# Performance work log

Measured on AMD Instinct MI355X. Metric: run time of the kernel, lower is better.

The kernel has to match this reference:

```python
import jax, jax.numpy as jnp
import numpy as np
from jax import lax

B, L, M, K, H, C = 16, 512, 2, 48, 128, 128
DIN = H * 2 + H + H + C  # 2 hidden layers + seq embed + mutant embed + edge feats = 640
H1, H2 = 512, 256
EPS = 1e-6


def _dist(Ca, mask, top_k=K, eps=EPS):
    # Ca: [B,L,3], mask: [B,L]
    m2 = mask[:, None, :] * mask[:, :, None]                                  # [B,L,L]
    D = m2 * jnp.sqrt(jnp.sum((Ca[:, :, None] - Ca[:, None, :]) ** 2, -1) + eps)
    D_adj = D + (1.0 - m2) * jnp.max(D, -1, keepdims=True)
    negD, E_idx = lax.top_k(-D_adj, top_k)                                    # smallest distances
    return -negD, E_idx


def reference(X, S, mask, chain_M, residue_idx, chain_encoding_all,
              mut_positions, mut_wildtype_AAs, mut_mutant_AAs, mut_ddGs, atom_mask,
              hid1, hid2, mpnn_embed, mpnn_edges, Ws, ln_g, ln_b,
              W1, b1, W2, b2, W3, b3):
    bidx = jnp.arange(B)[:, None]
    # _check_sequence_match: force S to wildtype at mutated positions
    S = S.at[bidx, mut_positions].set(mut_wildtype_AAs)
    X = jnp.nan_to_num(X, nan=0.0)

    # top-k neighbor graph from Ca coords
    _, E_idx = _dist(X[:, :, 1, :], mask)                                     # [B,L,K]

    # gather neighbor lists / edge features at mutation positions
    E_sel = jnp.take_along_axis(E_idx, mut_positions[:, :, None], axis=1)     # [B,M,K]
    Ed_sel = jnp.take_along_axis(mpnn_edges, mut_positions[:, :, None, None], axis=1)  # [B,M,K,C]

    # for each mutation, find edge to each other mutation (first match in neighbor list),
    # nanmean over others (missing -> excluded; all missing -> 0)
    edge_aggs = []
    for m in range(M):
        acc = jnp.zeros((B, C), mpnn_edges.dtype)
        cnt = jnp.zeros((B, 1), mpnn_edges.dtype)
        for o in range(M):
            if o == m:
                continue
            match = E_sel[:, m, :] == mut_positions[:, o, None]               # [B,K]
            has = jnp.any(match, -1)
            idx = jnp.argmax(match, -1)                                       # first occurrence
            edge = jnp.take_along_axis(Ed_sel[:, m], idx[:, None, None], axis=1)[:, 0]  # [B,C]
            acc = acc + edge * has[:, None].astype(edge.dtype)
            cnt = cnt + has[:, None].astype(edge.dtype)
        edge_aggs.append(acc / jnp.maximum(cnt, 1.0))
    edge_agg = jnp.stack(edge_aggs, axis=1)                                   # [B,M,C]

    # per-residue mpnn features and gathers at mutation positions
    h = jnp.concatenate([hid1, hid2, mpnn_embed], -1)                         # [B,L,384]
    g = jnp.take_along_axis(h, mut_positions[:, :, None], axis=1)             # [B,M,384]
    mut_e = Ws[mut_mutant_AAs]                                                # [B,M,H]
    emb = jnp.concatenate([g, mut_e, edge_agg], -1)                           # [B,M,DIN]

    # aggregate over valid mutations (padding has pos+wt+mut == 0)
    valid = ((mut_mutant_AAs + mut_wildtype_AAs + mut_positions) != 0).astype(emb.dtype)[:, :, None]
    agg = jnp.sum(emb * valid, axis=1) / jnp.maximum(jnp.sum(valid, axis=1), 1.0)  # [B,DIN]

    # ddg_out: LayerNorm -> (ReLU, Linear) x3
    mu = jnp.mean(agg, -1, keepdims=True)
    var = jnp.mean((agg - mu) ** 2, -1, keepdims=True)
    y = (agg - mu) / jnp.sqrt(var + 1e-5) * ln_g + ln_b
    y = jax.nn.relu(y) @ W1 + b1
    y = jax.nn.relu(y) @ W2 + b2
    y = jax.nn.relu(y) @ W3 + b3                                              # [B,1]
    return y


def setup_inputs() -> dict:
    key = jax.random.key(0)
    ks = jax.random.split(key, 16)
    f = lambda i, shp, s=1.0: jax.random.normal(ks[i], shp, dtype=jnp.float32) * s
    return {
        "X": f(0, (B, L, 4, 3), 5.0),
        "S": jax.random.randint(ks[1], (B, L), 0, 21),
        "mask": jnp.ones((B, L), jnp.float32),
        "chain_M": jnp.ones((B, L), jnp.float32),
        "residue_idx": jnp.tile(jnp.arange(L)[None, :], (B, 1)),
        "chain_encoding_all": jnp.zeros((B, L), jnp.int32),
        "mut_positions": jax.random.randint(ks[2], (B, M), 0, L),
        "mut_wildtype_AAs": jax.random.randint(ks[3], (B, M), 0, 21),
        "mut_mutant_AAs": jax.random.randint(ks[4], (B, M), 0, 21),
        "mut_ddGs": f(5, (B, M)),
        "atom_mask": jnp.ones((B, L, 4), jnp.float32),
        "hid1": f(6, (B, L, H)),
        "hid2": f(7, (B, L, H)),
        "mpnn_embed": f(8, (B, L, H)),
        "mpnn_edges": f(9, (B, L, K, C), 0.1),
        "Ws": f(10, (21, H), 0.02),
        "ln_g": jnp.ones((DIN,), jnp.float32),
        "ln_b": jnp.zeros((DIN,), jnp.float32),
        "W1": f(11, (DIN, H1), 0.02), "b1": jnp.zeros((H1,), jnp.float32),
        "W2": f(12, (H1, H2), 0.02), "b2": jnp.zeros((H2,), jnp.float32),
        "W3": f(13, (H2, 1), 0.02), "b3": jnp.zeros((1,), jnp.float32),
    }
```

## Files before the change

kernel.cpp:

```cpp
#include <hip/hip_runtime.h>
#include <hip/hip_bf16.h>

#define BB   16
#define LL   512
#define KNB  48
#define DIN_ 640
#define H1_  512
#define H2_  256
#define NT   512

__device__ __forceinline__ float nz(float x) { return x == x ? x : 0.0f; }

__device__ __forceinline__ float wave_sum(float v) {
  #pragma unroll
  for (int m = 32; m >= 1; m >>= 1) v += __shfl_xor(v, m);
  return v;
}

__global__ __launch_bounds__(NT) void k_fused(
    const float* __restrict__ X,
    const int*   __restrict__ mpos,
    const int*   __restrict__ mwt,
    const int*   __restrict__ mmut,
    const float* __restrict__ hid1,
    const float* __restrict__ hid2,
    const float* __restrict__ memb,
    const float* __restrict__ edges,
    const float* __restrict__ Wse,
    const float* __restrict__ ln_g,
    const float* __restrict__ ln_b,
    const float* __restrict__ W1,
    const float* __restrict__ b1,
    const float* __restrict__ W2,
    const float* __restrict__ b2,
    const float* __restrict__ W3,
    const float* __restrict__ b3,
    float* __restrict__ out)
{
  const int b   = blockIdx.x;
  const int t   = threadIdx.x;
  const int wid = t >> 6;

  __shared__ float s_x0[DIN_];
  __shared__ float s_x1[H1_];
  __shared__ float s_p2[NT];
  __shared__ float s_w[24];
  __shared__ int   s_cnt[16];

  const int p[2]  = { mpos[b * 2 + 0], mpos[b * 2 + 1] };
  const int mu[2] = { mmut[b * 2 + 0], mmut[b * 2 + 1] };
  const int wt[2] = { mwt[b * 2 + 0],  mwt[b * 2 + 1]  };

  float3 ca[2];
  #pragma unroll
  for (int m = 0; m < 2; ++m) {
    const float* a = X + (((size_t)(b * LL + p[m])) * 4 + 1) * 3;
    ca[m] = make_float3(nz(a[0]), nz(a[1]), nz(a[2]));
  }

  {
    const float* a = X + (((size_t)(b * LL + t)) * 4 + 1) * 3;
    const float jx = nz(a[0]), jy = nz(a[1]), jz = nz(a[2]);
    const float dx = ca[0].x - ca[1].x, dy = ca[0].y - ca[1].y, dz = ca[0].z - ca[1].z;
    const float dq = sqrtf(dx * dx + dy * dy + dz * dz + 1e-6f);

    const float e0x = jx - ca[0].x, e0y = jy - ca[0].y, e0z = jz - ca[0].z;
    const float d0  = sqrtf(e0x * e0x + e0y * e0y + e0z * e0z + 1e-6f);
    const float e1x = jx - ca[1].x, e1y = jy - ca[1].y, e1z = jz - ca[1].z;
    const float d1  = sqrtf(e1x * e1x + e1y * e1y + e1z * e1z + 1e-6f);

    const bool pr0 = (d0 < dq) || (d0 == dq && t < p[1]);
    const bool pr1 = (d1 < dq) || (d1 == dq && t < p[0]);
    const unsigned long long m0 = __ballot(pr0);
    const unsigned long long m1 = __ballot(pr1);
    if ((t & 63) == 0) {
      s_cnt[wid]     = __popcll(m0);
      s_cnt[8 + wid] = __popcll(m1);
    }
  }
  __syncthreads();

  int rk[2] = { 0, 0 };
  #pragma unroll
  for (int w = 0; w < 8; ++w) { rk[0] += s_cnt[w]; rk[1] += s_cnt[8 + w]; }

  const int v0 = ((p[0] + wt[0] + mu[0]) != 0) ? 1 : 0;
  const int v1 = ((p[1] + wt[1] + mu[1]) != 0) ? 1 : 0;
  const float denom = fmaxf((float)(v0 + v1), 1.0f);
  const int vv[2] = { v0, v1 };

  {
    const int d = t;
    if (true) {
      float v = 0.0f;
      #pragma unroll
      for (int m = 0; m < 2; ++m) {
        if (!vv[m]) continue;
        const int base = p[m];
        float e;
        if (d < 128)      e = hid1[(size_t)(b * LL + base) * 128 + d];
        else if (d < 256) e = hid2[(size_t)(b * LL + base) * 128 + (d - 128)];
        else if (d < 384) e = memb[(size_t)(b * LL + base) * 128 + (d - 256)];
        else              e = Wse[mu[m] * 128 + (d - 384)];
        v += e;
      }
      s_x0[d] = v / denom;
    }
    if (t < DIN_ - NT) {
      const int d = NT + t;
      float v = 0.0f;
      #pragma unroll
      for (int m = 0; m < 2; ++m) {
        if (!vv[m]) continue;
        if (rk[m] < KNB)
          v += edges[(((size_t)(b * LL + p[m])) * KNB + rk[m]) * 128 + (d - 512)];
      }
      s_x0[d] = v / denom;
    }
  }
  __syncthreads();

  float ps = s_x0[t] + ((t < DIN_ - NT) ? s_x0[NT + t] : 0.0f);
  ps = wave_sum(ps);
  if ((t & 63) == 0) s_w[wid] = ps;
  __syncthreads();
  float mu_ = 0.0f;
  #pragma unroll
  for (int w = 0; w < 8; ++w) mu_ += s_w[w];
  mu_ /= (float)DIN_;

  float z0 = s_x0[t] - mu_;
  float pv = z0 * z0;
  if (t < DIN_ - NT) { const float z1 = s_x0[NT + t] - mu_; pv += z1 * z1; }
  pv = wave_sum(pv);
  if ((t & 63) == 0) s_w[8 + wid] = pv;
  __syncthreads();
  float var = 0.0f;
  #pragma unroll
  for (int w = 0; w < 8; ++w) var += s_w[8 + w];
  var /= (float)DIN_;
  const float inv = 1.0f / sqrtf(var + 1e-5f);

  s_x0[t] = fmaxf((s_x0[t] - mu_) * inv * ln_g[t] + ln_b[t], 0.0f);
  if (t < DIN_ - NT)
    s_x0[NT + t] = fmaxf((s_x0[NT + t] - mu_) * inv * ln_g[NT + t] + ln_b[NT + t], 0.0f);
  __syncthreads();

  {
    const float* wp = W1 + t;
    float a0 = 0.f, a1 = 0.f, a2 = 0.f, a3 = 0.f,
          a4 = 0.f, a5 = 0.f, a6 = 0.f, a7 = 0.f;
    for (int r = 0; r < DIN_; r += 8) {
      a0 = fmaf(s_x0[r + 0], wp[(size_t)(r + 0) * H1_], a0);
      a1 = fmaf(s_x0[r + 1], wp[(size_t)(r + 1) * H1_], a1);
      a2 = fmaf(s_x0[r + 2], wp[(size_t)(r + 2) * H1_], a2);
      a3 = fmaf(s_x0[r + 3], wp[(size_t)(r + 3) * H1_], a3);
      a4 = fmaf(s_x0[r + 4], wp[(size_t)(r + 4) * H1_], a4);
      a5 = fmaf(s_x0[r + 5], wp[(size_t)(r + 5) * H1_], a5);
      a6 = fmaf(s_x0[r + 6], wp[(size_t)(r + 6) * H1_], a6);
      a7 = fmaf(s_x0[r + 7], wp[(size_t)(r + 7) * H1_], a7);
    }
    const float acc = ((a0 + a1) + (a2 + a3)) + ((a4 + a5) + (a6 + a7));
    s_x1[t] = fmaxf(acc + b1[t], 0.0f);
  }
  __syncthreads();

  {
    const int c = t & (H2_ - 1);
    const int h = t >> 8;
    const float* wp = W2 + (size_t)(h * 256) * H2_ + c;
    const float* xp = s_x1 + h * 256;
    float a0 = 0.f, a1 = 0.f, a2 = 0.f, a3 = 0.f;
    for (int r = 0; r < 256; r += 4) {
      a0 = fmaf(xp[r + 0], wp[(size_t)(r + 0) * H2_], a0);
      a1 = fmaf(xp[r + 1], wp[(size_t)(r + 1) * H2_], a1);
      a2 = fmaf(xp[r + 2], wp[(size_t)(r + 2) * H2_], a2);
      a3 = fmaf(xp[r + 3], wp[(size_t)(r + 3) * H2_], a3);
    }
    s_p2[t] = (a0 + a1) + (a2 + a3);
  }
  __syncthreads();

  float contrib = 0.0f;
  if (t < H2_)
    contrib = fmaxf(s_p2[t] + s_p2[t + 256] + b2[t], 0.0f) * W3[t];
  contrib = wave_sum(contrib);
  if ((t & 63) == 0) s_w[16 + wid] = contrib;
  __syncthreads();
  if (t == 0) {
    float s = 0.0f;
    #pragma unroll
    for (int w = 0; w < 8; ++w) s += s_w[16 + w];
    out[b] = s + b3[0];
  }
}

extern "C" void kernel_launch(void* const* d_in, const int* in_sizes, int n_in,
                              void* d_out, int out_size, void* d_ws, size_t ws_size,
                              hipStream_t stream) {
  const float* X     = (const float*)d_in[0];
  const int*   mpos  = (const int*)  d_in[6];
  const int*   mwt   = (const int*)  d_in[7];
  const int*   mmut  = (const int*)  d_in[8];
  const float* hid1  = (const float*)d_in[11];
  const float* hid2  = (const float*)d_in[12];
  const float* memb  = (const float*)d_in[13];
  const float* edges = (const float*)d_in[14];
  const float* Wse   = (const float*)d_in[15];
  const float* ln_g  = (const float*)d_in[16];
  const float* ln_b  = (const float*)d_in[17];
  const float* W1    = (const float*)d_in[18];
  const float* b1    = (const float*)d_in[19];
  const float* W2    = (const float*)d_in[20];
  const float* b2    = (const float*)d_in[21];
  const float* W3    = (const float*)d_in[22];
  const float* b3    = (const float*)d_in[23];

  float* out = (float*)d_out;

  k_fused<<<BB, NT, 0, stream>>>(X, mpos, mwt, mmut, hid1, hid2, memb, edges,
                                 Wse, ln_g, ln_b, W1, b1, W2, b2, W3, b3, out);
}
```

Measured before the change: 22.43 us.

## Double block size and split-K the MLP layers with float4 weight loads

Raises the block from 512 to 1024 threads and restructures the two dense layers. Each thread now computes four output columns over a slice of the reduction dimension with float4 weight loads, and the partial sums are reduced through a new shared buffer. The aim is a shorter serial dependency chain per thread and wider memory transactions in a latency-bound 16-block kernel. The cost is an extra shared-memory reduction pass and extra barriers, and only 16 blocks still run on a large GPU.

```diff
diff --git a/kernel.cpp b/kernel.cpp
--- a/kernel.cpp
+++ b/kernel.cpp
@@ -7,7 +7,7 @@
 #define DIN_ 640
 #define H1_  512
 #define H2_  256
-#define NT   512
+#define NT   1024
 
 __device__ __forceinline__ float nz(float x) { return x == x ? x : 0.0f; }
 
@@ -43,9 +43,9 @@
 
   __shared__ float s_x0[DIN_];
   __shared__ float s_x1[H1_];
-  __shared__ float s_p2[NT];
-  __shared__ float s_w[24];
-  __shared__ int   s_cnt[16];
+  __shared__ float s_fc[4096];
+  __shared__ float s_w[48];
+  __shared__ int   s_cnt[32];
 
   const int p[2]  = { mpos[b * 2 + 0], mpos[b * 2 + 1] };
   const int mu[2] = { mmut[b * 2 + 0], mmut[b * 2 + 1] };
@@ -59,138 +59,143 @@
   }
 
   {
-    const float* a = X + (((size_t)(b * LL + t)) * 4 + 1) * 3;
-    const float jx = nz(a[0]), jy = nz(a[1]), jz = nz(a[2]);
-    const float dx = ca[0].x - ca[1].x, dy = ca[0].y - ca[1].y, dz = ca[0].z - ca[1].z;
-    const float dq = sqrtf(dx * dx + dy * dy + dz * dz + 1e-6f);
-
-    const float e0x = jx - ca[0].x, e0y = jy - ca[0].y, e0z = jz - ca[0].z;
-    const float d0  = sqrtf(e0x * e0x + e0y * e0y + e0z * e0z + 1e-6f);
-    const float e1x = jx - ca[1].x, e1y = jy - ca[1].y, e1z = jz - ca[1].z;
-    const float d1  = sqrtf(e1x * e1x + e1y * e1y + e1z * e1z + 1e-6f);
-
-    const bool pr0 = (d0 < dq) || (d0 == dq && t < p[1]);
-    const bool pr1 = (d1 < dq) || (d1 == dq && t < p[0]);
+    bool pr0 = false, pr1 = false;
+    if (t < LL) {
+      const float* a = X + (((size_t)(b * LL + t)) * 4 + 1) * 3;
+      const float jx = nz(a[0]), jy = nz(a[1]), jz = nz(a[2]);
+      const float dx = ca[0].x - ca[1].x, dy = ca[0].y - ca[1].y, dz = ca[0].z - ca[1].z;
+      const float dq = sqrtf(dx * dx + dy * dy + dz * dz + 1e-6f);
+
+      const float e0x = jx - ca[0].x, e0y = jy - ca[0].y, e0z = jz - ca[0].z;
+      const float d0  = sqrtf(e0x * e0x + e0y * e0y + e0z * e0z + 1e-6f);
+      const float e1x = jx - ca[1].x, e1y = jy - ca[1].y, e1z = jz - ca[1].z;
+      const float d1  = sqrtf(e1x * e1x + e1y * e1y + e1z * e1z + 1e-6f);
+
+      pr0 = (d0 < dq) || (d0 == dq && t < p[1]);
+      pr1 = (d1 < dq) || (d1 == dq && t < p[0]);
+    }
     const unsigned long long m0 = __ballot(pr0);
     const unsigned long long m1 = __ballot(pr1);
     if ((t & 63) == 0) {
-      s_cnt[wid]     = __popcll(m0);
-      s_cnt[8 + wid] = __popcll(m1);
+      s_cnt[wid]      = __popcll(m0);
+      s_cnt[16 + wid] = __popcll(m1);
     }
   }
   __syncthreads();
 
   int rk[2] = { 0, 0 };
   #pragma unroll
-  for (int w = 0; w < 8; ++w) { rk[0] += s_cnt[w]; rk[1] += s_cnt[8 + w]; }
+  for (int w = 0; w < 16; ++w) { rk[0] += s_cnt[w]; rk[1] += s_cnt[16 + w]; }
 
   const int v0 = ((p[0] + wt[0] + mu[0]) != 0) ? 1 : 0;
   const int v1 = ((p[1] + wt[1] + mu[1]) != 0) ? 1 : 0;
   const float denom = fmaxf((float)(v0 + v1), 1.0f);
   const int vv[2] = { v0, v1 };
 
-  {
+  if (t < DIN_) {
     const int d = t;
-    if (true) {
-      float v = 0.0f;
-      #pragma unroll
-      for (int m = 0; m < 2; ++m) {
-        if (!vv[m]) continue;
-        const int base = p[m];
-        float e;
-        if (d < 128)      e = hid1[(size_t)(b * LL + base) * 128 + d];
-        else if (d < 256) e = hid2[(size_t)(b * LL + base) * 128 + (d - 128)];
-        else if (d < 384) e = memb[(size_t)(b * LL + base) * 128 + (d - 256)];
-        else              e = Wse[mu[m] * 128 + (d - 384)];
-        v += e;
-      }
-      s_x0[d] = v / denom;
-    }
-    if (t < DIN_ - NT) {
-      const int d = NT + t;
-      float v = 0.0f;
-      #pragma unroll
-      for (int m = 0; m < 2; ++m) {
-        if (!vv[m]) continue;
-        if (rk[m] < KNB)
-          v += edges[(((size_t)(b * LL + p[m])) * KNB + rk[m]) * 128 + (d - 512)];
-      }
-      s_x0[d] = v / denom;
-    }
-  }
-  __syncthreads();
-
-  float ps = s_x0[t] + ((t < DIN_ - NT) ? s_x0[NT + t] : 0.0f);
+    float v = 0.0f;
+    #pragma unroll
+    for (int m = 0; m < 2; ++m) {
+      if (!vv[m]) continue;
+      const int base = p[m];
+      float e;
+      if (d < 128)      e = hid1[(size_t)(b * LL + base) * 128 + d];
+      else if (d < 256) e = hid2[(size_t)(b * LL + base) * 128 + (d - 128)];
+      else if (d < 384) e = memb[(size_t)(b * LL + base) * 128 + (d - 256)];
+      else if (d < 512) e = Wse[mu[m] * 128 + (d - 384)];
+      else              e = (rk[m] < KNB)
+                              ? edges[(((size_t)(b * LL + base)) * KNB + rk[m]) * 128 + (d - 512)]
+                              : 0.0f;
+      v += e;
+    }
+    s_x0[d] = v / denom;
+  }
+  __syncthreads();
+
+  float ps = (t < DIN_) ? s_x0[t] : 0.0f;
   ps = wave_sum(ps);
   if ((t & 63) == 0) s_w[wid] = ps;
   __syncthreads();
   float mu_ = 0.0f;
   #pragma unroll
-  for (int w = 0; w < 8; ++w) mu_ += s_w[w];
+  for (int w = 0; w < 16; ++w) mu_ += s_w[w];
   mu_ /= (float)DIN_;
 
-  float z0 = s_x0[t] - mu_;
-  float pv = z0 * z0;
-  if (t < DIN_ - NT) { const float z1 = s_x0[NT + t] - mu_; pv += z1 * z1; }
+  float pv = 0.0f;
+  if (t < DIN_) { const float z = s_x0[t] - mu_; pv = z * z; }
   pv = wave_sum(pv);
-  if ((t & 63) == 0) s_w[8 + wid] = pv;
+  if ((t & 63) == 0) s_w[16 + wid] = pv;
   __syncthreads();
   float var = 0.0f;
   #pragma unroll
-  for (int w = 0; w < 8; ++w) var += s_w[8 + w];
+  for (int w = 0; w < 16; ++w) var += s_w[16 + w];
   var /= (float)DIN_;
   const float inv = 1.0f / sqrtf(var + 1e-5f);
 
-  s_x0[t] = fmaxf((s_x0[t] - mu_) * inv * ln_g[t] + ln_b[t], 0.0f);
-  if (t < DIN_ - NT)
-    s_x0[NT + t] = fmaxf((s_x0[NT + t] - mu_) * inv * ln_g[NT + t] + ln_b[NT + t], 0.0f);
+  if (t < DIN_)
+    s_x0[t] = fmaxf((s_x0[t] - mu_) * inv * ln_g[t] + ln_b[t], 0.0f);
   __syncthreads();
 
   {
-    const float* wp = W1 + t;
-    float a0 = 0.f, a1 = 0.f, a2 = 0.f, a3 = 0.f,
-          a4 = 0.f, a5 = 0.f, a6 = 0.f, a7 = 0.f;
-    for (int r = 0; r < DIN_; r += 8) {
-      a0 = fmaf(s_x0[r + 0], wp[(size_t)(r + 0) * H1_], a0);
-      a1 = fmaf(s_x0[r + 1], wp[(size_t)(r + 1) * H1_], a1);
-      a2 = fmaf(s_x0[r + 2], wp[(size_t)(r + 2) * H1_], a2);
-      a3 = fmaf(s_x0[r + 3], wp[(size_t)(r + 3) * H1_], a3);
-      a4 = fmaf(s_x0[r + 4], wp[(size_t)(r + 4) * H1_], a4);
-      a5 = fmaf(s_x0[r + 5], wp[(size_t)(r + 5) * H1_], a5);
-      a6 = fmaf(s_x0[r + 6], wp[(size_t)(r + 6) * H1_], a6);
-      a7 = fmaf(s_x0[r + 7], wp[(size_t)(r + 7) * H1_], a7);
-    }
-    const float acc = ((a0 + a1) + (a2 + a3)) + ((a4 + a5) + (a6 + a7));
+    const int g  = t & 127;
+    const int sl = t >> 7;
+    const int r0 = sl * 80;
+    float4 a = make_float4(0.f, 0.f, 0.f, 0.f);
+    #pragma unroll 8
+    for (int i = 0; i < 80; ++i) {
+      const int r = r0 + i;
+      const float xv = s_x0[r];
+      const float4 w = reinterpret_cast<const float4*>(W1 + (size_t)r * H1_)[g];
+      a.x = fmaf(xv, w.x, a.x);
+      a.y = fmaf(xv, w.y, a.y);
+      a.z = fmaf(xv, w.z, a.z);
+      a.w = fmaf(xv, w.w, a.w);
+    }
+    reinterpret_cast<float4*>(s_fc)[sl * 128 + g] = a;
+  }
+  __syncthreads();
+  if (t < H1_) {
+    float acc = 0.0f;
+    #pragma unroll
+    for (int sl = 0; sl < 8; ++sl) acc += s_fc[sl * 512 + t];
     s_x1[t] = fmaxf(acc + b1[t], 0.0f);
   }
   __syncthreads();
 
   {
-    const int c = t & (H2_ - 1);
-    const int h = t >> 8;
-    const float* wp = W2 + (size_t)(h * 256) * H2_ + c;
-    const float* xp = s_x1 + h * 256;
-    float a0 = 0.f, a1 = 0.f, a2 = 0.f, a3 = 0.f;
-    for (int r = 0; r < 256; r += 4) {
-      a0 = fmaf(xp[r + 0], wp[(size_t)(r + 0) * H2_], a0);
-      a1 = fmaf(xp[r + 1], wp[(size_t)(r + 1) * H2_], a1);
-      a2 = fmaf(xp[r + 2], wp[(size_t)(r + 2) * H2_], a2);
-      a3 = fmaf(xp[r + 3], wp[(size_t)(r + 3) * H2_], a3);
-    }
-    s_p2[t] = (a0 + a1) + (a2 + a3);
+    const int g  = t & 63;
+    const int sl = t >> 6;
+    const int r0 = sl * 32;
+    float4 a = make_float4(0.f, 0.f, 0.f, 0.f);
+    #pragma unroll 8
+    for (int i = 0; i < 32; ++i) {
+      const int r = r0 + i;
+      const float xv = s_x1[r];
+      const float4 w = reinterpret_cast<const float4*>(W2 + (size_t)r * H2_)[g];
+      a.x = fmaf(xv, w.x, a.x);
+      a.y = fmaf(xv, w.y, a.y);
+      a.z = fmaf(xv, w.z, a.z);
+      a.w = fmaf(xv, w.w, a.w);
+    }
+    reinterpret_cast<float4*>(s_fc)[sl * 64 + g] = a;
   }
   __syncthreads();
 
   float contrib = 0.0f;
-  if (t < H2_)
-    contrib = fmaxf(s_p2[t] + s_p2[t + 256] + b2[t], 0.0f) * W3[t];
+  if (t < H2_) {
+    float acc = 0.0f;
+    #pragma unroll
+    for (int sl = 0; sl < 16; ++sl) acc += s_fc[sl * 256 + t];
+    contrib = fmaxf(acc + b2[t], 0.0f) * W3[t];
+  }
   contrib = wave_sum(contrib);
-  if ((t & 63) == 0) s_w[16 + wid] = contrib;
+  if ((t & 63) == 0) s_w[32 + wid] = contrib;
   __syncthreads();
   if (t == 0) {
     float s = 0.0f;
     #pragma unroll
-    for (int w = 0; w < 8; ++w) s += s_w[16 + w];
+    for (int w = 0; w < 16; ++w) s += s_w[32 + w];
     out[b] = s + b3[0];
   }
 }
```

New measurement: 22.05 us. Within noise of the previous version (-1.7%).
